# Kernel optimization log

Measured on AMD Instinct MI355X. Metric: run time of the kernel, lower is better.

Reference implementation:

```python
import jax, jax.numpy as jnp
import numpy as np

TOKENS_PER_LAYER = 16  # v in rearrange 'b l (a v) -> b l a v'


def setup_inputs() -> dict:
    key = jax.random.key(0)
    k1, k2 = jax.random.split(key)
    vocab, embed_dim = 1024, 256
    x = jax.random.normal(k1, (64, 32, embed_dim * TOKENS_PER_LAYER), dtype=jnp.float32)
    # nn.Embedding init: uniform(-1/vocab, 1/vocab)
    emb_weight = jax.random.uniform(k2, (vocab, embed_dim), dtype=jnp.float32,
                                    minval=-1.0 / vocab, maxval=1.0 / vocab)
    return {"x": x, "emb_weight": emb_weight}


def reference(x, emb_weight):
    v = TOKENS_PER_LAYER
    b, l, av = x.shape
    a = av // v  # embed_dim
    # rearrange 'b l (a v) -> b l a v'
    z = x.reshape(b, l, a, v)
    # rearrange 'b l a v -> (b l v) a'
    z_flat = z.transpose(0, 1, 3, 2).reshape(b * l * v, a)
    # pairwise squared L2 distance via sum-of-squares + GEMM: [N, vocab]
    dist = (jnp.sum(z_flat * z_flat, axis=1, keepdims=True)
            + jnp.sum(emb_weight * emb_weight, axis=1)
            - 2.0 * (z_flat @ emb_weight.T))
    tokens = jnp.argmin(dist, axis=-1)  # [N] int
    # embedding gather, then rearrange '(b l v) e -> b l e v'
    z_q = emb_weight[tokens].reshape(b, l, v, a).transpose(0, 1, 3, 2)
    # straight-through decoder input: z + sg(z_q - z)
    decoder_input = z + jax.lax.stop_gradient(z_q - z)
    tokens = tokens.reshape(b, l, v)
    return z_q, decoder_input, tokens
```

## Files before the change

### kernel.cpp

```cpp
#include <hip/hip_runtime.h>


#define A_DIM 256
#define VOCAB 1024
#define NROWS 32768
#define ZQ_ELEMS ((size_t)8388608)
#define TAU_C 3.0e-4f
#define TAU_F 2.0e-4f

typedef _Float16 f16x8 __attribute__((ext_vector_type(8)));
typedef float f32x4 __attribute__((ext_vector_type(4)));

#define WS_EHT   ((size_t)0)
#define WS_ZH    ((size_t)524288)
#define WS_ESQ   ((size_t)17301504)
#define WS_ZSQ   ((size_t)17305600)
#define WS_TOK   ((size_t)17436672)
#define WS_PLIST ((size_t)17567744)
#define WS_FLIST ((size_t)18092032)
#define WS_CNT   ((size_t)18223104)
#define WS_NEED  ((size_t)18223232)


__global__ __launch_bounds__(256) void prep_e_kernel(const float* __restrict__ emb,
                                                     float* __restrict__ esq,
                                                     _Float16* __restrict__ eht,
                                                     int* __restrict__ cnt) {
    const int tid = threadIdx.x;
    if (blockIdx.x == 0 && tid < 2) cnt[tid] = 0;
    const int j = blockIdx.x * 16 + (tid & 15);
    const int sub = tid >> 4;
    const float4* row = (const float4*)(emb + (size_t)j * A_DIM);
    #pragma unroll
    for (int t = 0; t < 2; ++t) {
        int kb = sub * 2 + t;
        float4 e0 = row[kb * 2], e1 = row[kb * 2 + 1];
        f16x8 h;
        h[0] = (_Float16)e0.x; h[1] = (_Float16)e0.y; h[2] = (_Float16)e0.z; h[3] = (_Float16)e0.w;
        h[4] = (_Float16)e1.x; h[5] = (_Float16)e1.y; h[6] = (_Float16)e1.z; h[7] = (_Float16)e1.w;
        *(f16x8*)(eht + ((size_t)kb * 1024 + j) * 8) = h;
    }
    if (sub == 0) {
        double s = 0.0;
        #pragma unroll 4
        for (int t = 0; t < A_DIM / 4; ++t) {
            float4 f = row[t];
            float sx = f.x * f.x, sy = f.y * f.y, sz = f.z * f.z, sw = f.w * f.w;
            s += (double)sx + (double)sy + (double)sz + (double)sw;
        }
        esq[j] = (float)s;
    }
}

__global__ __launch_bounds__(256) void prep_z_kernel(const float* __restrict__ x,
                                                     _Float16* __restrict__ zh,
                                                     float* __restrict__ zsq) {
    __shared__ float raw[A_DIM * 17];
    const int tid = threadIdx.x;
    const int bl = blockIdx.x;
    #pragma unroll
    for (int t = 0; t < 4; ++t) {
        int f4 = tid * 4 + t * 1024;
        float4 val = *(const float4*)(x + (size_t)bl * 4096 + f4);
        int a = f4 >> 4, v0 = f4 & 15;
        raw[a * 17 + v0 + 0] = val.x;
        raw[a * 17 + v0 + 1] = val.y;
        raw[a * 17 + v0 + 2] = val.z;
        raw[a * 17 + v0 + 3] = val.w;
    }
    __syncthreads();
    #pragma unroll
    for (int t = 0; t < 16; ++t) {
        int f = tid + t * 256;
        int v = f >> 8, a = f & 255;
        zh[((size_t)bl * 16 + v) * 256 + a] = (_Float16)raw[a * 17 + v];
    }
    if (tid < 16) {
        double s = 0.0;
        for (int a = 0; a < A_DIM; ++a) {
            float zf = raw[a * 17 + tid];
            float z2 = zf * zf;
            s += (double)z2;
        }
        zsq[bl * 16 + tid] = (float)s;
    }
}

__global__ __launch_bounds__(256) void mfma_kernel(const _Float16* __restrict__ zh,
                                                   const _Float16* __restrict__ eht,
                                                   const float* __restrict__ esq_g,
                                                   int* __restrict__ tok,
                                                   int4* __restrict__ plist,
                                                   int* __restrict__ flist,
                                                   int* __restrict__ cnt,
                                                   float* __restrict__ out) {
    __shared__ float t3buf[2][32][6];
    const int tid = threadIdx.x;
    const int w = tid >> 6;
    const int lane = tid & 63;
    const int q = lane >> 4;
    const int ln = lane & 15;
    const int g = w & 1;
    const int h = w >> 1;
    const int row0 = blockIdx.x * 32 + g * 16;
    const int cbase = h * 512;

    f16x8 afr[8];
    #pragma unroll
    for (int kt = 0; kt < 8; ++kt)
        afr[kt] = *(const f16x8*)(zh + (size_t)(row0 + ln) * 256 + kt * 32 + q * 8);

    const f16x8* ep[8];
    #pragma unroll
    for (int kt = 0; kt < 8; ++kt)
        ep[kt] = (const f16x8*)(eht + ((size_t)(kt * 4 + q) * 1024 + cbase + ln) * 8);

    float tv1[4], tv2[4], tv3[4];
    int   ti1[4], ti2[4], ti3[4];
    #pragma unroll
    for (int s = 0; s < 4; ++s) {
        tv1[s] = 3.0e38f; tv2[s] = 3.0e38f; tv3[s] = 3.0e38f;
        ti1[s] = 0; ti2[s] = 0; ti3[s] = 0;
    }

    for (int ch = 0; ch < 32; ++ch) {
        f16x8 bfr[8];
        #pragma unroll
        for (int kt = 0; kt < 8; ++kt)
            bfr[kt] = ep[kt][(size_t)ch * 16];
        f32x4 a0 = (f32x4){0.f, 0.f, 0.f, 0.f};
        f32x4 a1 = (f32x4){0.f, 0.f, 0.f, 0.f};
        #pragma unroll
        for (int kt = 0; kt < 4; ++kt)
            a0 = __builtin_amdgcn_mfma_f32_16x16x32_f16(afr[kt], bfr[kt], a0, 0, 0, 0);
        #pragma unroll
        for (int kt = 4; kt < 8; ++kt)
            a1 = __builtin_amdgcn_mfma_f32_16x16x32_f16(afr[kt], bfr[kt], a1, 0, 0, 0);
        const int cand = cbase + ch * 16 + ln;
        float es = esq_g[cand];
        #pragma unroll
        for (int reg = 0; reg < 4; ++reg) {
            float s = fmaf(-2.0f, a0[reg] + a1[reg], es);
            if (s < tv3[reg]) {
                if (s < tv2[reg]) {
                    tv3[reg] = tv2[reg]; ti3[reg] = ti2[reg];
                    if (s < tv1[reg]) {
                        tv2[reg] = tv1[reg]; ti2[reg] = ti1[reg];
                        tv1[reg] = s; ti1[reg] = cand;
                    } else { tv2[reg] = s; ti2[reg] = cand; }
                } else { tv3[reg] = s; ti3[reg] = cand; }
            }
        }
    }

    #pragma unroll
    for (int slot = 0; slot < 4; ++slot) {
        float v1 = tv1[slot], v2 = tv2[slot], v3 = tv3[slot];
        int i1 = ti1[slot], i2 = ti2[slot], i3 = ti3[slot];
        #pragma unroll
        for (int m = 1; m <= 8; m <<= 1) {
            float ov1 = __shfl_xor(v1, m); int oi1 = __shfl_xor(i1, m);
            float ov2 = __shfl_xor(v2, m); int oi2 = __shfl_xor(i2, m);
            float ov3 = __shfl_xor(v3, m); int oi3 = __shfl_xor(i3, m);
            #define INS3(ov, oi)                                                         \
                if (ov < v3 || (ov == v3 && oi < i3)) {                                  \
                    if (ov < v2 || (ov == v2 && oi < i2)) {                              \
                        v3 = v2; i3 = i2;                                                \
                        if (ov < v1 || (ov == v1 && oi < i1)) {                          \
                            v2 = v1; i2 = i1; v1 = ov; i1 = oi;                          \
                        } else { v2 = ov; i2 = oi; }                                     \
                    } else { v3 = ov; i3 = oi; }                                         \
                }
            INS3(ov1, oi1)
            INS3(ov2, oi2)
            INS3(ov3, oi3)
            #undef INS3
        }
        if (ln == 0) {
            int rl = g * 16 + q * 4 + slot;
            float* hp = &t3buf[h][rl][0];
            hp[0] = v1; hp[1] = __int_as_float(i1);
            hp[2] = v2; hp[3] = __int_as_float(i2);
            hp[4] = v3; hp[5] = __int_as_float(i3);
        }
    }
    __syncthreads();

    if (tid < 32) {
        const float* h0 = &t3buf[0][tid][0];
        const float* h1 = &t3buf[1][tid][0];
        float v1 = h0[0]; int i1 = __float_as_int(h0[1]);
        float v2 = h0[2]; int i2 = __float_as_int(h0[3]);
        float v3 = h0[4]; int i3 = __float_as_int(h0[5]);
        #pragma unroll
        for (int e = 0; e < 3; ++e) {
            float ov = h1[2 * e]; int oi = __float_as_int(h1[2 * e + 1]);
            if (ov < v3 || (ov == v3 && oi < i3)) {
                if (ov < v2 || (ov == v2 && oi < i2)) {
                    v3 = v2; i3 = i2;
                    if (ov < v1 || (ov == v1 && oi < i1)) {
                        v2 = v1; i2 = i1; v1 = ov; i1 = oi;
                    } else { v2 = ov; i2 = oi; }
                } else { v3 = ov; i3 = oi; }
            }
        }
        int row = blockIdx.x * 32 + tid;
        tok[row] = i1;
        out[2 * ZQ_ELEMS + (size_t)row] = (float)i1;
        if (v2 - v1 <= TAU_C) {
            if (v3 - v1 > TAU_C) {
                int p = atomicAdd(&cnt[0], 1) & (NROWS - 1);
                plist[p] = make_int4(row, i1, i2, 0);
            } else {
                int p = atomicAdd(&cnt[1], 1) & (NROWS - 1);
                flist[p] = row;
            }
        }
    }
}

__global__ __launch_bounds__(256) void rescan2_kernel(const float* __restrict__ x,
                                                      const float* __restrict__ emb,
                                                      const float* __restrict__ esq,
                                                      const float* __restrict__ zsq,
                                                      int* __restrict__ tok,
                                                      const int4* __restrict__ plist,
                                                      const int* __restrict__ flist,
                                                      const int* __restrict__ cnt,
                                                      float* __restrict__ out) {
    __shared__ float zrow[A_DIM];
    __shared__ float wv[4];
    __shared__ int   wi[4];
    const int tid = threadIdx.x;
    const int w = tid >> 6, lane = tid & 63;

    {
        const int nw = gridDim.x * 4;
        const int gw = blockIdx.x * 4 + w;
        const int np = min(cnt[0], NROWS);
        for (int i = gw; i < np; i += nw) {
            int4 e = plist[i];
            const int r = e.x, c1 = e.y, c2 = e.z;
            const float* xr = x + (size_t)(r >> 4) * 4096 + (r & 15);
            const float* e1 = emb + (size_t)c1 * A_DIM;
            const float* e2 = emb + (size_t)c2 * A_DIM;
            double d1 = 0.0, d2 = 0.0;
            #pragma unroll
            for (int k = 0; k < 4; ++k) {
                int a = lane + k * 64;
                double zv = (double)xr[a * 16];
                d1 = fma(zv, (double)e1[a], d1);
                d2 = fma(zv, (double)e2[a], d2);
            }
            #pragma unroll
            for (int m = 1; m < 64; m <<= 1) {
                d1 += __shfl_xor(d1, m);
                d2 += __shfl_xor(d2, m);
            }
            if (lane == 0) {
                float zq = zsq[r];
                float A1 = zq + esq[c1];
                float D1 = (float)(2.0 * d1);
                float s1 = A1 - D1;
                float A2 = zq + esq[c2];
                float D2 = (float)(2.0 * d2);
                float s2 = A2 - D2;
                int bi = (s2 < s1 || (s2 == s1 && c2 < c1)) ? c2 : c1;
                tok[r] = bi;
                out[2 * ZQ_ELEMS + (size_t)r] = (float)bi;
            }
        }
    }

    const int nf = min(cnt[1], NROWS);
    for (int i = blockIdx.x; i < nf; i += gridDim.x) {
        const int r = flist[i];
        __syncthreads();
        zrow[tid] = x[(size_t)(r >> 4) * 4096 + (size_t)tid * 16 + (r & 15)];
        __syncthreads();

        const float4* e0 = (const float4*)(emb + (size_t)tid * 4 * A_DIM);
        double d0 = 0.0, d1 = 0.0, d2 = 0.0, d3 = 0.0;
        #pragma unroll 8
        for (int k4 = 0; k4 < A_DIM / 4; ++k4) {
            float4 zf = *(const float4*)&zrow[k4 * 4];
            double z0 = (double)zf.x, z1 = (double)zf.y;
            double z2 = (double)zf.z, z3 = (double)zf.w;
            float4 f0 = e0[k4];
            float4 f1 = e0[64 + k4];
            float4 f2 = e0[128 + k4];
            float4 f3 = e0[192 + k4];
            d0 = fma((double)f0.x, z0, d0); d0 = fma((double)f0.y, z1, d0);
            d0 = fma((double)f0.z, z2, d0); d0 = fma((double)f0.w, z3, d0);
            d1 = fma((double)f1.x, z0, d1); d1 = fma((double)f1.y, z1, d1);
            d1 = fma((double)f1.z, z2, d1); d1 = fma((double)f1.w, z3, d1);
            d2 = fma((double)f2.x, z0, d2); d2 = fma((double)f2.y, z1, d2);
            d2 = fma((double)f2.z, z2, d2); d2 = fma((double)f2.w, z3, d2);
            d3 = fma((double)f3.x, z0, d3); d3 = fma((double)f3.y, z1, d3);
            d3 = fma((double)f3.z, z2, d3); d3 = fma((double)f3.w, z3, d3);
        }
        const float zq = zsq[r];
        float bv = 3.0e38f; int bi = 0;
        double dd[4] = {d0, d1, d2, d3};
        #pragma unroll
        for (int cc = 0; cc < 4; ++cc) {
            int c = tid * 4 + cc;
            float A = zq + esq[c];
            float D = (float)(2.0 * dd[cc]);
            float s = A - D;
            if (s < bv) { bv = s; bi = c; }
        }
        #pragma unroll
        for (int m = 1; m < 64; m <<= 1) {
            float ov = __shfl_xor(bv, m); int oi = __shfl_xor(bi, m);
            if (ov < bv || (ov == bv && oi < bi)) { bv = ov; bi = oi; }
        }
        if (lane == 0) { wv[w] = bv; wi[w] = bi; }
        __syncthreads();
        if (tid == 0) {
            float BV = wv[0]; int BI = wi[0];
            #pragma unroll
            for (int t = 1; t < 4; ++t)
                if (wv[t] < BV || (wv[t] == BV && wi[t] < BI)) { BV = wv[t]; BI = wi[t]; }
            tok[r] = BI;
            out[2 * ZQ_ELEMS + (size_t)r] = (float)BI;
        }
    }
}

__global__ __launch_bounds__(256) void gather_kernel(const float* __restrict__ emb,
                                                     const int* __restrict__ tok,
                                                     float* __restrict__ out) {
    __shared__ int t16[16];
    const int tid = threadIdx.x;
    const int bl = blockIdx.x;
    if (tid < 16) t16[tid] = tok[bl * 16 + tid];
    __syncthreads();
    const int a = tid;
    __align__(16) float h[16];
    #pragma unroll
    for (int v = 0; v < 16; ++v) h[v] = emb[(size_t)t16[v] * A_DIM + a];
    size_t base = ((size_t)bl * A_DIM + a) * 16;
    float4* p0 = (float4*)(out + base);
    float4* p1 = (float4*)(out + ZQ_ELEMS + base);
    #pragma unroll
    for (int qq = 0; qq < 4; ++qq) {
        float4 val = *(float4*)&h[qq * 4];
        p0[qq] = val;
        p1[qq] = val;
    }
}


__global__ __launch_bounds__(256) void prep_f(const float* __restrict__ emb,
                                              float* __restrict__ e_sq32) {
    int j = blockIdx.x * 256 + threadIdx.x;
    if (j < VOCAB) {
        const float4* row = (const float4*)(emb + (size_t)j * A_DIM);
        double s = 0.0;
        #pragma unroll 4
        for (int t = 0; t < A_DIM / 4; ++t) {
            float4 f = row[t];
            float sx = f.x * f.x, sy = f.y * f.y, sz = f.z * f.z, sw = f.w * f.w;
            s += (double)sx + (double)sy + (double)sz + (double)sw;
        }
        e_sq32[j] = (float)s;
    }
}

#define FBM 64
#define FBN 256
#define FBK 32
struct SmemF {
    union {
        struct { float zs[FBK][FBM]; float es[FBK][FBN]; };
        float4 mbuf[FBM][32];
        struct { double zrow[A_DIM]; float rbest[256]; int ridx[256]; };
    };
    double zsqp_s[4][FBM];
    float  zsq[FBM];
    int    tok[FBM];
    int    flagrows[FBM];
    int    nflag;
};

__global__ __launch_bounds__(256, 2) void main_f(const float* __restrict__ x,
                                                 const float* __restrict__ emb,
                                                 const float* __restrict__ e_sq32,
                                                 float* __restrict__ out) {
    __shared__ SmemF sm;
    const int tid = threadIdx.x;
    const int tx = tid & 31;
    const int ty = tid >> 5;
    const int blk = blockIdx.x;
    const int row0 = blk * FBM;
    const int bl0 = row0 >> 4;
    const int zrow_id = tid & 63;
    const int zq4     = tid >> 6;

    if (tid == 0) sm.nflag = 0;
    float v1[8], v2[8];
    int   i1[8], i2[8];
    #pragma unroll
    for (int r = 0; r < 8; ++r) { v1[r] = 3.0e38f; v2[r] = 3.0e38f; i1[r] = 0; i2[r] = 0; }
    double zsqp = 0.0;
    float4 zpf[2];
    float4 epf[8];
    for (int ct = 0; ct < VOCAB / FBN; ++ct) {
        float acc[8][8];
        #pragma unroll
        for (int rr = 0; rr < 8; ++rr)
            #pragma unroll
            for (int cc = 0; cc < 8; ++cc) acc[rr][cc] = 0.0f;
        for (int kt = 0; kt < A_DIM / FBK; ++kt) {
            if (kt == 0) {
                #pragma unroll
                for (int t = 0; t < 2; ++t) {
                    int f = tid + t * 256;
                    int v4 = f & 3, g = (f >> 2) & 3, kk = f >> 4;
                    zpf[t] = *(const float4*)(x + (size_t)(bl0 + g) * 4096 + (kt * FBK + kk) * 16 + v4 * 4);
                }
                #pragma unroll
                for (int t = 0; t < 8; ++t) {
                    int f = tid + t * 256;
                    int c = f & 255, k4 = f >> 8;
                    epf[t] = *(const float4*)(emb + (size_t)(ct * FBN + c) * A_DIM + kt * FBK + k4 * 4);
                }
            }
            __syncthreads();
            #pragma unroll
            for (int t = 0; t < 2; ++t) {
                int f = tid + t * 256;
                int v4 = f & 3, g = (f >> 2) & 3, kk = f >> 4;
                *(float4*)&sm.zs[kk][g * 16 + v4 * 4] = zpf[t];
            }
            #pragma unroll
            for (int t = 0; t < 8; ++t) {
                int f = tid + t * 256;
                int c = f & 255, k4 = f >> 8;
                sm.es[k4 * 4 + 0][c] = epf[t].x;
                sm.es[k4 * 4 + 1][c] = epf[t].y;
                sm.es[k4 * 4 + 2][c] = epf[t].z;
                sm.es[k4 * 4 + 3][c] = epf[t].w;
            }
            __syncthreads();
            if (kt + 1 < A_DIM / FBK) {
                #pragma unroll
                for (int t = 0; t < 2; ++t) {
                    int f = tid + t * 256;
                    int v4 = f & 3, g = (f >> 2) & 3, kk = f >> 4;
                    zpf[t] = *(const float4*)(x + (size_t)(bl0 + g) * 4096 + ((kt + 1) * FBK + kk) * 16 + v4 * 4);
                }
                #pragma unroll
                for (int t = 0; t < 8; ++t) {
                    int f = tid + t * 256;
                    int c = f & 255, k4 = f >> 8;
                    epf[t] = *(const float4*)(emb + (size_t)(ct * FBN + c) * A_DIM + (kt + 1) * FBK + k4 * 4);
                }
            }
            if (ct == 0 && (kt >> 1) == zq4) {
                #pragma unroll
                for (int kk = 0; kk < FBK; ++kk) {
                    float zf = sm.zs[kk][zrow_id];
                    float zf2 = zf * zf;
                    zsqp += (double)zf2;
                }
            }
            #pragma unroll 2
            for (int kk = 0; kk < FBK; ++kk) {
                float4 za = *(float4*)&sm.zs[kk][ty * 4];
                float4 zb = *(float4*)&sm.zs[kk][32 + ty * 4];
                float4 ea = *(float4*)&sm.es[kk][tx * 4];
                float4 eb = *(float4*)&sm.es[kk][128 + tx * 4];
                float zv[8] = {za.x, za.y, za.z, za.w, zb.x, zb.y, zb.z, zb.w};
                float ev[8] = {ea.x, ea.y, ea.z, ea.w, eb.x, eb.y, eb.z, eb.w};
                #pragma unroll
                for (int rr = 0; rr < 8; ++rr)
                    #pragma unroll
                    for (int cc = 0; cc < 8; ++cc)
                        acc[rr][cc] = fmaf(zv[rr], ev[cc], acc[rr][cc]);
            }
        }
        if (ct == 0) {
            sm.zsqp_s[zq4][zrow_id] = zsqp;
            __syncthreads();
            if (tid < FBM)
                sm.zsq[tid] = (float)(sm.zsqp_s[0][tid] + sm.zsqp_s[1][tid]
                                    + sm.zsqp_s[2][tid] + sm.zsqp_s[3][tid]);
            __syncthreads();
        }
        float esqv[8];
        #pragma unroll
        for (int cc = 0; cc < 8; ++cc) {
            int c = ct * FBN + (cc >> 2) * 128 + tx * 4 + (cc & 3);
            esqv[cc] = e_sq32[c];
        }
        #pragma unroll
        for (int rr = 0; rr < 8; ++rr) {
            int R = (rr >> 2) * 32 + ty * 4 + (rr & 3);
            float zq = sm.zsq[R];
            #pragma unroll
            for (int cc = 0; cc < 8; ++cc) {
                int c = ct * FBN + (cc >> 2) * 128 + tx * 4 + (cc & 3);
                float A = zq + esqv[cc];
                float s = fmaf(-2.0f, acc[rr][cc], A);
                if (s < v1[rr]) { v2[rr] = v1[rr]; i2[rr] = i1[rr]; v1[rr] = s; i1[rr] = c; }
                else if (s < v2[rr]) { v2[rr] = s; i2[rr] = c; }
            }
        }
    }
    __syncthreads();
    #pragma unroll
    for (int rr = 0; rr < 8; ++rr) {
        int r = (rr >> 2) * 32 + ty * 4 + (rr & 3);
        float4 m;
        m.x = v1[rr]; m.y = __int_as_float(i1[rr]);
        m.z = v2[rr]; m.w = __int_as_float(i2[rr]);
        sm.mbuf[r][tx] = m;
    }
    __syncthreads();
    if (tid < FBM) {
        int r = tid;
        float V1 = 3.0e38f, V2 = 3.0e38f;
        int I1 = 0, I2 = 0;
        for (int t = 0; t < 32; ++t) {
            float4 m = sm.mbuf[r][t];
            float a1 = m.x; int a1i = __float_as_int(m.y);
            float a2 = m.z; int a2i = __float_as_int(m.w);
            if (a1 < V1 || (a1 == V1 && a1i < I1)) { V2 = V1; I2 = I1; V1 = a1; I1 = a1i; }
            else if (a1 < V2 || (a1 == V2 && a1i < I2)) { V2 = a1; I2 = a1i; }
            if (a2 < V1 || (a2 == V1 && a2i < I1)) { V2 = V1; I2 = I1; V1 = a2; I1 = a2i; }
            else if (a2 < V2 || (a2 == V2 && a2i < I2)) { V2 = a2; I2 = a2i; }
        }
        sm.tok[r] = I1;
        if (V2 - V1 <= TAU_F) {
            int pos = atomicAdd(&sm.nflag, 1);
            sm.flagrows[pos] = r;
        }
    }
    __syncthreads();
    const int nf = sm.nflag;
    for (int i = 0; i < nf; ++i) {
        const int rl = sm.flagrows[i];
        const int bl = bl0 + (rl >> 4);
        const int v  = rl & 15;
        const float zqrow = sm.zsq[rl];
        sm.zrow[tid] = (double)x[(size_t)bl * 4096 + (size_t)tid * 16 + v];
        __syncthreads();
        float bv = 3.0e38f; int bi = 0;
        #pragma unroll
        for (int cc = 0; cc < 4; ++cc) {
            int c = tid * 4 + cc;
            const float4* er = (const float4*)(emb + (size_t)c * A_DIM);
            double dot = 0.0;
            #pragma unroll 8
            for (int k4 = 0; k4 < A_DIM / 4; ++k4) {
                float4 f = er[k4];
                dot = fma((double)f.x, sm.zrow[k4 * 4 + 0], dot);
                dot = fma((double)f.y, sm.zrow[k4 * 4 + 1], dot);
                dot = fma((double)f.z, sm.zrow[k4 * 4 + 2], dot);
                dot = fma((double)f.w, sm.zrow[k4 * 4 + 3], dot);
            }
            float A = zqrow + e_sq32[c];
            float D = (float)(2.0 * dot);
            float s = A - D;
            if (s < bv) { bv = s; bi = c; }
        }
        sm.rbest[tid] = bv; sm.ridx[tid] = bi;
        __syncthreads();
        if (tid == 0) {
            float BV = sm.rbest[0]; int BI = sm.ridx[0];
            for (int t = 1; t < 256; ++t) {
                float vv = sm.rbest[t];
                if (vv < BV) { BV = vv; BI = sm.ridx[t]; }
            }
            sm.tok[rl] = BI;
        }
        __syncthreads();
    }
    if (tid < FBM) {
        out[2 * ZQ_ELEMS + (size_t)(row0 + tid)] = (float)sm.tok[tid];
    }
    __syncthreads();
    const int a = tid;
    for (int g = 0; g < 4; ++g) {
        __align__(16) float h[16];
        #pragma unroll
        for (int v = 0; v < 16; ++v) {
            h[v] = emb[(size_t)sm.tok[g * 16 + v] * A_DIM + a];
        }
        size_t base = ((size_t)(bl0 + g) * A_DIM + a) * 16;
        float4* p0 = (float4*)(out + base);
        float4* p1 = (float4*)(out + ZQ_ELEMS + base);
        #pragma unroll
        for (int qq = 0; qq < 4; ++qq) {
            float4 val = *(float4*)&h[qq * 4];
            p0[qq] = val;
            p1[qq] = val;
        }
    }
}

extern "C" void kernel_launch(void* const* d_in, const int* in_sizes, int n_in,
                              void* d_out, int out_size, void* d_ws, size_t ws_size,
                              hipStream_t stream) {
    (void)in_sizes; (void)n_in; (void)out_size;
    const float* x   = (const float*)d_in[0];
    const float* emb = (const float*)d_in[1];
    float* out = (float*)d_out;
    char* ws = (char*)d_ws;

    if (ws_size >= WS_NEED) {
        _Float16* eht = (_Float16*)(ws + WS_EHT);
        _Float16* zh  = (_Float16*)(ws + WS_ZH);
        float* esq    = (float*)(ws + WS_ESQ);
        float* zsq    = (float*)(ws + WS_ZSQ);
        int* tok      = (int*)(ws + WS_TOK);
        int4* plist   = (int4*)(ws + WS_PLIST);
        int* flist    = (int*)(ws + WS_FLIST);
        int* cnt      = (int*)(ws + WS_CNT);

        prep_e_kernel<<<64, 256, 0, stream>>>(emb, esq, eht, cnt);
        prep_z_kernel<<<2048, 256, 0, stream>>>(x, zh, zsq);
        mfma_kernel<<<1024, 256, 0, stream>>>(zh, eht, esq, tok, plist, flist, cnt, out);
        rescan2_kernel<<<256, 256, 0, stream>>>(x, emb, esq, zsq, tok, plist, flist, cnt, out);
        gather_kernel<<<2048, 256, 0, stream>>>(emb, tok, out);
    } else {
        float* e_sq32 = (float*)ws;
        prep_f<<<4, 256, 0, stream>>>(emb, e_sq32);
        main_f<<<512, 256, 0, stream>>>(x, emb, e_sq32, out);
    }
}
```

Baseline: 230.8 us.

## Fuse prep kernels and merge MFMA, rescan and gather into one kernel

Merges the two prep kernels into one launch, with extra blocks handling the embedding conversion. The MFMA argmin, the near-tie rescans and the embedding gather now run in a single kernel that keeps per-row tokens and tie classes in shared memory. This removes three launches, the global token and candidate lists, and the atomic counters. The cost is that full rescans now run inside the block that found the tie, serialised per row, so a block with many ties can stall and the load across blocks becomes uneven.

```diff
diff --git a/kernel.cpp b/kernel.cpp
--- a/kernel.cpp
+++ b/kernel.cpp
@@ -15,48 +15,43 @@
 #define WS_ZH    ((size_t)524288)
 #define WS_ESQ   ((size_t)17301504)
 #define WS_ZSQ   ((size_t)17305600)
-#define WS_TOK   ((size_t)17436672)
-#define WS_PLIST ((size_t)17567744)
-#define WS_FLIST ((size_t)18092032)
-#define WS_CNT   ((size_t)18223104)
-#define WS_NEED  ((size_t)18223232)
-
-
-__global__ __launch_bounds__(256) void prep_e_kernel(const float* __restrict__ emb,
-                                                     float* __restrict__ esq,
-                                                     _Float16* __restrict__ eht,
-                                                     int* __restrict__ cnt) {
-    const int tid = threadIdx.x;
-    if (blockIdx.x == 0 && tid < 2) cnt[tid] = 0;
-    const int j = blockIdx.x * 16 + (tid & 15);
-    const int sub = tid >> 4;
-    const float4* row = (const float4*)(emb + (size_t)j * A_DIM);
-    #pragma unroll
-    for (int t = 0; t < 2; ++t) {
-        int kb = sub * 2 + t;
-        float4 e0 = row[kb * 2], e1 = row[kb * 2 + 1];
-        f16x8 h;
-        h[0] = (_Float16)e0.x; h[1] = (_Float16)e0.y; h[2] = (_Float16)e0.z; h[3] = (_Float16)e0.w;
-        h[4] = (_Float16)e1.x; h[5] = (_Float16)e1.y; h[6] = (_Float16)e1.z; h[7] = (_Float16)e1.w;
-        *(f16x8*)(eht + ((size_t)kb * 1024 + j) * 8) = h;
-    }
-    if (sub == 0) {
-        double s = 0.0;
-        #pragma unroll 4
-        for (int t = 0; t < A_DIM / 4; ++t) {
-            float4 f = row[t];
-            float sx = f.x * f.x, sy = f.y * f.y, sz = f.z * f.z, sw = f.w * f.w;
-            s += (double)sx + (double)sy + (double)sz + (double)sw;
-        }
-        esq[j] = (float)s;
-    }
-}
-
-__global__ __launch_bounds__(256) void prep_z_kernel(const float* __restrict__ x,
-                                                     _Float16* __restrict__ zh,
-                                                     float* __restrict__ zsq) {
+#define WS_NEED  ((size_t)17436672)
+
+
+__global__ __launch_bounds__(256) void prep_fused(const float* __restrict__ x,
+                                                  const float* __restrict__ emb,
+                                                  _Float16* __restrict__ zh,
+                                                  float* __restrict__ zsq,
+                                                  float* __restrict__ esq,
+                                                  _Float16* __restrict__ eht) {
     __shared__ float raw[A_DIM * 17];
     const int tid = threadIdx.x;
+    if (blockIdx.x >= 2048) {
+        const int blk = blockIdx.x - 2048;
+        const int j = blk * 16 + (tid & 15);
+        const int sub = tid >> 4;
+        const float4* row = (const float4*)(emb + (size_t)j * A_DIM);
+        #pragma unroll
+        for (int t = 0; t < 2; ++t) {
+            int kb = sub * 2 + t;
+            float4 e0 = row[kb * 2], e1 = row[kb * 2 + 1];
+            f16x8 hh;
+            hh[0] = (_Float16)e0.x; hh[1] = (_Float16)e0.y; hh[2] = (_Float16)e0.z; hh[3] = (_Float16)e0.w;
+            hh[4] = (_Float16)e1.x; hh[5] = (_Float16)e1.y; hh[6] = (_Float16)e1.z; hh[7] = (_Float16)e1.w;
+            *(f16x8*)(eht + ((size_t)kb * 1024 + j) * 8) = hh;
+        }
+        if (sub == 0) {
+            double s = 0.0;
+            #pragma unroll 4
+            for (int t = 0; t < A_DIM / 4; ++t) {
+                float4 f = row[t];
+                float sx = f.x * f.x, sy = f.y * f.y, sz = f.z * f.z, sw = f.w * f.w;
+                s += (double)sx + (double)sy + (double)sz + (double)sw;
+            }
+            esq[j] = (float)s;
+        }
+        return;
+    }
     const int bl = blockIdx.x;
     #pragma unroll
     for (int t = 0; t < 4; ++t) {
@@ -86,22 +81,26 @@
     }
 }
 
-__global__ __launch_bounds__(256) void mfma_kernel(const _Float16* __restrict__ zh,
+__global__ __launch_bounds__(256) void mega_kernel(const _Float16* __restrict__ zh,
                                                    const _Float16* __restrict__ eht,
                                                    const float* __restrict__ esq_g,
-                                                   int* __restrict__ tok,
-                                                   int4* __restrict__ plist,
-                                                   int* __restrict__ flist,
-                                                   int* __restrict__ cnt,
+                                                   const float* __restrict__ zsq,
+                                                   const float* __restrict__ x,
+                                                   const float* __restrict__ emb,
                                                    float* __restrict__ out) {
     __shared__ float t3buf[2][32][6];
+    __shared__ float zrow[A_DIM];
+    __shared__ float wv[4];
+    __shared__ int   wi[4];
+    __shared__ int rowtok[32], rowcls[32], rowc1[32], rowc2[32];
+
     const int tid = threadIdx.x;
-    const int w = tid >> 6;
+    const int wq = tid >> 6;
     const int lane = tid & 63;
     const int q = lane >> 4;
     const int ln = lane & 15;
-    const int g = w & 1;
-    const int h = w >> 1;
+    const int g = wq & 1;
+    const int h = wq >> 1;
     const int row0 = blockIdx.x * 32 + g * 16;
     const int cbase = h * 512;
 
@@ -204,81 +203,21 @@
                 } else { v3 = ov; i3 = oi; }
             }
         }
-        int row = blockIdx.x * 32 + tid;
-        tok[row] = i1;
-        out[2 * ZQ_ELEMS + (size_t)row] = (float)i1;
-        if (v2 - v1 <= TAU_C) {
-            if (v3 - v1 > TAU_C) {
-                int p = atomicAdd(&cnt[0], 1) & (NROWS - 1);
-                plist[p] = make_int4(row, i1, i2, 0);
-            } else {
-                int p = atomicAdd(&cnt[1], 1) & (NROWS - 1);
-                flist[p] = row;
-            }
-        }
-    }
-}
-
-__global__ __launch_bounds__(256) void rescan2_kernel(const float* __restrict__ x,
-                                                      const float* __restrict__ emb,
-                                                      const float* __restrict__ esq,
-                                                      const float* __restrict__ zsq,
-                                                      int* __restrict__ tok,
-                                                      const int4* __restrict__ plist,
-                                                      const int* __restrict__ flist,
-                                                      const int* __restrict__ cnt,
-                                                      float* __restrict__ out) {
-    __shared__ float zrow[A_DIM];
-    __shared__ float wv[4];
-    __shared__ int   wi[4];
-    const int tid = threadIdx.x;
-    const int w = tid >> 6, lane = tid & 63;
-
-    {
-        const int nw = gridDim.x * 4;
-        const int gw = blockIdx.x * 4 + w;
-        const int np = min(cnt[0], NROWS);
-        for (int i = gw; i < np; i += nw) {
-            int4 e = plist[i];
-            const int r = e.x, c1 = e.y, c2 = e.z;
-            const float* xr = x + (size_t)(r >> 4) * 4096 + (r & 15);
-            const float* e1 = emb + (size_t)c1 * A_DIM;
-            const float* e2 = emb + (size_t)c2 * A_DIM;
-            double d1 = 0.0, d2 = 0.0;
-            #pragma unroll
-            for (int k = 0; k < 4; ++k) {
-                int a = lane + k * 64;
-                double zv = (double)xr[a * 16];
-                d1 = fma(zv, (double)e1[a], d1);
-                d2 = fma(zv, (double)e2[a], d2);
-            }
-            #pragma unroll
-            for (int m = 1; m < 64; m <<= 1) {
-                d1 += __shfl_xor(d1, m);
-                d2 += __shfl_xor(d2, m);
-            }
-            if (lane == 0) {
-                float zq = zsq[r];
-                float A1 = zq + esq[c1];
-                float D1 = (float)(2.0 * d1);
-                float s1 = A1 - D1;
-                float A2 = zq + esq[c2];
-                float D2 = (float)(2.0 * d2);
-                float s2 = A2 - D2;
-                int bi = (s2 < s1 || (s2 == s1 && c2 < c1)) ? c2 : c1;
-                tok[r] = bi;
-                out[2 * ZQ_ELEMS + (size_t)r] = (float)bi;
-            }
-        }
-    }
-
-    const int nf = min(cnt[1], NROWS);
-    for (int i = blockIdx.x; i < nf; i += gridDim.x) {
-        const int r = flist[i];
+        rowtok[tid] = i1;
+        rowc1[tid] = i1;
+        rowc2[tid] = i2;
+        int cls = 0;
+        if (v2 - v1 <= TAU_C) cls = (v3 - v1 > TAU_C) ? 1 : 2;
+        rowcls[tid] = cls;
+    }
+    __syncthreads();
+
+    for (int rl = 0; rl < 32; ++rl) {
+        if (rowcls[rl] != 2) continue;
+        const int r = blockIdx.x * 32 + rl;
         __syncthreads();
         zrow[tid] = x[(size_t)(r >> 4) * 4096 + (size_t)tid * 16 + (r & 15)];
         __syncthreads();
-
         const float4* e0 = (const float4*)(emb + (size_t)tid * 4 * A_DIM);
         double d0 = 0.0, d1 = 0.0, d2 = 0.0, d3 = 0.0;
         #pragma unroll 8
@@ -305,7 +244,7 @@
         #pragma unroll
         for (int cc = 0; cc < 4; ++cc) {
             int c = tid * 4 + cc;
-            float A = zq + esq[c];
+            float A = zq + esq_g[c];
             float D = (float)(2.0 * dd[cc]);
             float s = A - D;
             if (s < bv) { bv = s; bi = c; }
@@ -315,40 +254,71 @@
             float ov = __shfl_xor(bv, m); int oi = __shfl_xor(bi, m);
             if (ov < bv || (ov == bv && oi < bi)) { bv = ov; bi = oi; }
         }
-        if (lane == 0) { wv[w] = bv; wi[w] = bi; }
+        if (lane == 0) { wv[wq] = bv; wi[wq] = bi; }
         __syncthreads();
         if (tid == 0) {
             float BV = wv[0]; int BI = wi[0];
             #pragma unroll
             for (int t = 1; t < 4; ++t)
                 if (wv[t] < BV || (wv[t] == BV && wi[t] < BI)) { BV = wv[t]; BI = wi[t]; }
-            tok[r] = BI;
-            out[2 * ZQ_ELEMS + (size_t)r] = (float)BI;
-        }
-    }
-}
-
-__global__ __launch_bounds__(256) void gather_kernel(const float* __restrict__ emb,
-                                                     const int* __restrict__ tok,
-                                                     float* __restrict__ out) {
-    __shared__ int t16[16];
-    const int tid = threadIdx.x;
-    const int bl = blockIdx.x;
-    if (tid < 16) t16[tid] = tok[bl * 16 + tid];
-    __syncthreads();
+            rowtok[rl] = BI;
+        }
+    }
+
+    for (int rl = wq; rl < 32; rl += 4) {
+        if (rowcls[rl] != 1) continue;
+        const int r = blockIdx.x * 32 + rl;
+        const int c1 = rowc1[rl], c2 = rowc2[rl];
+        const float* xr = x + (size_t)(r >> 4) * 4096 + (r & 15);
+        const float* e1 = emb + (size_t)c1 * A_DIM;
+        const float* e2 = emb + (size_t)c2 * A_DIM;
+        double d1 = 0.0, d2 = 0.0;
+        #pragma unroll
+        for (int k = 0; k < 4; ++k) {
+            int a = lane + k * 64;
+            double zv = (double)xr[a * 16];
+            d1 = fma(zv, (double)e1[a], d1);
+            d2 = fma(zv, (double)e2[a], d2);
+        }
+        #pragma unroll
+        for (int m = 1; m < 64; m <<= 1) {
+            d1 += __shfl_xor(d1, m);
+            d2 += __shfl_xor(d2, m);
+        }
+        if (lane == 0) {
+            float zq = zsq[r];
+            float A1 = zq + esq_g[c1];
+            float D1 = (float)(2.0 * d1);
+            float s1 = A1 - D1;
+            float A2 = zq + esq_g[c2];
+            float D2 = (float)(2.0 * d2);
+            float s2 = A2 - D2;
+            int bi = (s2 < s1 || (s2 == s1 && c2 < c1)) ? c2 : c1;
+            rowtok[rl] = bi;
+        }
+    }
+    __syncthreads();
+
     const int a = tid;
-    __align__(16) float h[16];
-    #pragma unroll
-    for (int v = 0; v < 16; ++v) h[v] = emb[(size_t)t16[v] * A_DIM + a];
-    size_t base = ((size_t)bl * A_DIM + a) * 16;
-    float4* p0 = (float4*)(out + base);
-    float4* p1 = (float4*)(out + ZQ_ELEMS + base);
-    #pragma unroll
-    for (int qq = 0; qq < 4; ++qq) {
-        float4 val = *(float4*)&h[qq * 4];
-        p0[qq] = val;
-        p1[qq] = val;
-    }
+    #pragma unroll
+    for (int gg = 0; gg < 2; ++gg) {
+        const int bl = blockIdx.x * 2 + gg;
+        __align__(16) float hbuf[16];
+        #pragma unroll
+        for (int v = 0; v < 16; ++v)
+            hbuf[v] = emb[(size_t)rowtok[gg * 16 + v] * A_DIM + a];
+        size_t base = ((size_t)bl * A_DIM + a) * 16;
+        float4* p0 = (float4*)(out + base);
+        float4* p1 = (float4*)(out + ZQ_ELEMS + base);
+        #pragma unroll
+        for (int qq = 0; qq < 4; ++qq) {
+            float4 val = *(float4*)&hbuf[qq * 4];
+            p0[qq] = val;
+            p1[qq] = val;
+        }
+    }
+    if (tid < 32)
+        out[2 * ZQ_ELEMS + (size_t)(blockIdx.x * 32 + tid)] = (float)rowtok[tid];
 }
 
 
@@ -615,16 +585,9 @@
         _Float16* zh  = (_Float16*)(ws + WS_ZH);
         float* esq    = (float*)(ws + WS_ESQ);
         float* zsq    = (float*)(ws + WS_ZSQ);
-        int* tok      = (int*)(ws + WS_TOK);
-        int4* plist   = (int4*)(ws + WS_PLIST);
-        int* flist    = (int*)(ws + WS_FLIST);
-        int* cnt      = (int*)(ws + WS_CNT);
-
-        prep_e_kernel<<<64, 256, 0, stream>>>(emb, esq, eht, cnt);
-        prep_z_kernel<<<2048, 256, 0, stream>>>(x, zh, zsq);
-        mfma_kernel<<<1024, 256, 0, stream>>>(zh, eht, esq, tok, plist, flist, cnt, out);
-        rescan2_kernel<<<256, 256, 0, stream>>>(x, emb, esq, zsq, tok, plist, flist, cnt, out);
-        gather_kernel<<<2048, 256, 0, stream>>>(emb, tok, out);
+
+        prep_fused<<<2112, 256, 0, stream>>>(x, emb, zh, zsq, esq, eht);
+        mega_kernel<<<1024, 256, 0, stream>>>(zh, eht, esq, zsq, x, emb, out);
     } else {
         float* e_sq32 = (float*)ws;
         prep_f<<<4, 256, 0, stream>>>(emb, e_sq32);
```

Result: slower. 280.0 us (+21.3%).
